# Kernel tuning notes

Measured on AMD Instinct MI355X. Metric: run time of the kernel, lower is better.

Reference implementation:

```python
import jax, jax.numpy as jnp
import numpy as np

D_MODEL = 512
NUM_HEADS = 8
DFF = 2048
DEPTH = D_MODEL // NUM_HEADS
EPS = 1e-6


def setup_inputs() -> dict:
    key = jax.random.key(0)
    ks = jax.random.split(key, 16)
    B, S, d = 4, 2048, D_MODEL
    s = 1.0 / np.sqrt(d)
    inp = {
        'x': jax.random.normal(ks[0], (B, S, d), jnp.float32),
        'Wq': jax.random.normal(ks[1], (d, d), jnp.float32) * s,
        'bq': jnp.zeros((d,), jnp.float32),
        'Wk': jax.random.normal(ks[2], (d, d), jnp.float32) * s,
        'bk': jnp.zeros((d,), jnp.float32),
        'Wv': jax.random.normal(ks[3], (d, d), jnp.float32) * s,
        'bv': jnp.zeros((d,), jnp.float32),
        'Wo': jax.random.normal(ks[4], (d, d), jnp.float32) * s,
        'bo': jnp.zeros((d,), jnp.float32),
        'W1': jax.random.normal(ks[5], (d, DFF), jnp.float32) * s,
        'b1': jnp.zeros((DFF,), jnp.float32),
        'W2': jax.random.normal(ks[6], (DFF, d), jnp.float32) * (1.0 / np.sqrt(DFF)),
        'b2': jnp.zeros((d,), jnp.float32),
        'g1': jnp.ones((d,), jnp.float32),
        'be1': jnp.zeros((d,), jnp.float32),
        'g2': jnp.ones((d,), jnp.float32),
        'be2': jnp.zeros((d,), jnp.float32),
    }
    return inp


def _layer_norm(x, g, b):
    mu = jnp.mean(x, axis=-1, keepdims=True)
    var = jnp.mean(jnp.square(x - mu), axis=-1, keepdims=True)
    return (x - mu) * jax.lax.rsqrt(var + EPS) * g + b


def _split_heads(t, B, S):
    # (B,S,d_model) -> (B,H,S,depth)
    return t.reshape(B, S, NUM_HEADS, DEPTH).transpose(0, 2, 1, 3)


def reference(x, Wq, bq, Wk, bk, Wv, bv, Wo, bo, W1, b1, W2, b2, g1, be1, g2, be2):
    B, S, d = x.shape
    q = _split_heads(x @ Wq + bq, B, S)
    k = _split_heads(x @ Wk + bk, B, S)
    v = _split_heads(x @ Wv + bv, B, S)
    # tf.keras Attention default: UNscaled dot product
    scores = jnp.einsum('bhqd,bhkd->bhqk', q, k)
    attn = jax.nn.softmax(scores, axis=-1)
    ctx = jnp.einsum('bhqk,bhkd->bhqd', attn, v)
    ctx = ctx.transpose(0, 2, 1, 3).reshape(B, S, d)
    attn_out = ctx @ Wo + bo
    x1 = _layer_norm(x + attn_out, g1, be1)
    ff = jax.nn.relu(x1 @ W1 + b1) @ W2 + b2
    return _layer_norm(x1 + ff, g2, be2)
```

## Files before the change

### kernel.cpp

```cpp
#include <hip/hip_runtime.h>
#include <hip/hip_bf16.h>
#include <math.h>

#define NH 8
#define DEPTH 64
#define SEQ 2048
#define BATCH 4
#define DM 512
#define DFFN 2048
#define NROWS (BATCH * SEQ)

typedef __attribute__((ext_vector_type(8))) short  s16x8;
typedef __attribute__((ext_vector_type(4))) short  s16x4;
typedef __attribute__((ext_vector_type(4))) float  f32x4;

__device__ __forceinline__ float bf2f(unsigned short u) {
    union { unsigned int i; float f; } c;
    c.i = ((unsigned int)u) << 16;
    return c.f;
}
__device__ __forceinline__ unsigned short f2bf_rn(float x) {
    union { float f; unsigned int i; } c; c.f = x;
    unsigned int r = c.i + 0x7fffu + ((c.i >> 16) & 1u);
    return (unsigned short)(r >> 16);
}
__device__ __forceinline__ float ldin(const void* p, long i, int f32) {
    return f32 ? ((const float*)p)[i] : bf2f(((const unsigned short*)p)[i]);
}
__device__ __forceinline__ float4 ld4in(const void* p, long i, int f32) {
    if (f32) return *reinterpret_cast<const float4*>((const float*)p + i);
    ushort4 u = *reinterpret_cast<const ushort4*>((const unsigned short*)p + i);
    return make_float4(bf2f(u.x), bf2f(u.y), bf2f(u.z), bf2f(u.w));
}

__global__ void detect_kernel(const void* w, int* flag) {
    if (threadIdx.x == 0 && blockIdx.x == 0) {
        const unsigned short* u = (const unsigned short*)w;
        int isf32 = 0;
        for (int i = 0; i < 2048; ++i) {
            float v = fabsf(bf2f(u[i]));
            if (!(v < 1e3f)) { isf32 = 1; break; }
        }
        *flag = isf32;
    }
}

__global__ __launch_bounds__(256)
void asplit_kernel(const void* __restrict__ A, unsigned short* __restrict__ hi,
                   unsigned short* __restrict__ lo, const int* __restrict__ dflag)
{
    const int f32 = *dflag;
    long i = ((long)blockIdx.x * 256 + threadIdx.x) * 4;
    float4 v = ld4in(A, i, f32);
    float xs[4] = {v.x, v.y, v.z, v.w};
    s16x4 h, l;
    #pragma unroll
    for (int j = 0; j < 4; ++j) {
        unsigned short hh = f2bf_rn(xs[j]);
        h[j] = (short)hh;
        l[j] = (short)f2bf_rn(xs[j] - bf2f(hh));
    }
    *reinterpret_cast<s16x4*>(hi + i) = h;
    *reinterpret_cast<s16x4*>(lo + i) = l;
}

__global__ __launch_bounds__(256)
void wsplit_kernel(const void* __restrict__ W, unsigned short* __restrict__ whiT,
                   unsigned short* __restrict__ wloT, int K, int N,
                   const int* __restrict__ dflag)
{
    const int f32 = *dflag;
    __shared__ float T[64][65];
    const int k0 = blockIdx.x * 64, n0 = blockIdx.y * 64;
    const int tid = threadIdx.x;
    #pragma unroll
    for (int i = 0; i < 4; ++i) {
        int k = (tid >> 4) + i * 16;
        int n = (tid & 15) * 4;
        float4 w4 = ld4in(W, (long)(k0 + k) * N + n0 + n, f32);
        T[k][n] = w4.x; T[k][n + 1] = w4.y; T[k][n + 2] = w4.z; T[k][n + 3] = w4.w;
    }
    __syncthreads();
    #pragma unroll
    for (int i = 0; i < 4; ++i) {
        int n = (tid >> 4) + i * 16;
        int k = (tid & 15) * 4;
        s16x4 hv, lv;
        #pragma unroll
        for (int j = 0; j < 4; ++j) {
            float x = T[k + j][n];
            unsigned short h = f2bf_rn(x);
            hv[j] = (short)h;
            lv[j] = (short)f2bf_rn(x - bf2f(h));
        }
        *reinterpret_cast<s16x4*>(&whiT[(long)(n0 + n) * K + k0 + k]) = hv;
        *reinterpret_cast<s16x4*>(&wloT[(long)(n0 + n) * K + k0 + k]) = lv;
    }
}

__global__ __launch_bounds__(256)
void vtrans_kernel(const unsigned short* __restrict__ vin,
                   unsigned short* __restrict__ vout)
{
    __shared__ unsigned short T[64][72];
    const int tid = threadIdx.x;
    const int s0 = blockIdx.x * 64;
    const int bh = blockIdx.y;
    const unsigned short* src = vin + ((long)bh * SEQ + s0) * DEPTH;
    #pragma unroll
    for (int i = 0; i < 2; ++i) {
        int f = tid + i * 256, row = f >> 3, oct = f & 7;
        *reinterpret_cast<s16x8*>(&T[row][oct * 8]) =
            *reinterpret_cast<const s16x8*>(src + (long)row * DEPTH + oct * 8);
    }
    __syncthreads();
    unsigned short* dst = vout + (long)bh * DEPTH * SEQ + s0;
    #pragma unroll
    for (int i = 0; i < 2; ++i) {
        int f = tid + i * 256;
        int d = f >> 3, oct = f & 7;
        s16x8 v;
        #pragma unroll
        for (int e = 0; e < 8; ++e) v[e] = (short)T[oct * 8 + e][d];
        *reinterpret_cast<s16x8*>(dst + (long)d * SEQ + oct * 8) = v;
    }
}

#define ASTR 40
template<int BM, int AMODE, int OMODE, bool RELU, int TERMS>
__global__ __launch_bounds__(256)
void mfma_gemm(const void* __restrict__ A, const void* __restrict__ A2,
               const unsigned short* __restrict__ WhiT,
               const unsigned short* __restrict__ WloT,
               const void* __restrict__ bias, const void* __restrict__ bias2,
               const void* __restrict__ bias3,
               void* __restrict__ C, void* __restrict__ C2,
               void* __restrict__ C3, void* __restrict__ C4,
               void* __restrict__ C5,
               int M, int N, int K, const int* __restrict__ dflag)
{
    constexpr int FM  = BM / 32;
    constexpr int CPT = BM / 64;
    constexpr int BLO = (TERMS == 3) ? 128 : 1;
    const int f32 = *dflag;
    __shared__ unsigned short Ahi[BM][ASTR], Alo[BM][ASTR];
    __shared__ unsigned short Bhi[128][ASTR];
    __shared__ unsigned short Blo[BLO][ASTR];

    const int tid  = threadIdx.x;
    const int wave = tid >> 6, lane = tid & 63;
    const int lr = lane & 15, lg = lane >> 4;
    const int wm = (wave >> 1) * (BM / 2), wn = (wave & 1) * 64;
    const int bx = blockIdx.x, by = blockIdx.y;

    const int srB = tid >> 1;
    const int shB = (tid & 1) * 16;

    s16x8 arh[CPT], arl[CPT];
    auto loadA = [&](int kt) {
        const unsigned short* ah = (const unsigned short*)A;
        const unsigned short* al = (const unsigned short*)A2;
        #pragma unroll
        for (int i = 0; i < CPT; ++i) {
            int c = tid * CPT + i;
            int row = c >> 2, q = c & 3;
            int gm = by * BM + row;
            int gk = kt + q * 8;
            long base;
            if (AMODE == 3) {
                int b = gm / SEQ, s = gm % SEQ;
                int hh = gk >> 6, dep = gk & 63;
                base = ((long)(b * NH + hh) * SEQ + s) * DEPTH + dep;
            } else {
                base = (long)gm * K + gk;
            }
            arh[i] = *reinterpret_cast<const s16x8*>(ah + base);
            arl[i] = *reinterpret_cast<const s16x8*>(al + base);
        }
    };
    s16x8 brh[2], brl[2];
    auto loadB = [&](int kt) {
        long base = (long)(bx * 128 + srB) * K + kt + shB;
        brh[0] = *reinterpret_cast<const s16x8*>(&WhiT[base]);
        brh[1] = *reinterpret_cast<const s16x8*>(&WhiT[base + 8]);
        if constexpr (TERMS == 3) {
            brl[0] = *reinterpret_cast<const s16x8*>(&WloT[base]);
            brl[1] = *reinterpret_cast<const s16x8*>(&WloT[base + 8]);
        }
    };

    f32x4 acc[FM][4];
    #pragma unroll
    for (int i = 0; i < FM; ++i)
        #pragma unroll
        for (int j = 0; j < 4; ++j) acc[i][j] = (f32x4){0.f, 0.f, 0.f, 0.f};

    loadA(0);
    loadB(0);

    for (int kt = 0; kt < K; kt += 32) {
        #pragma unroll
        for (int i = 0; i < CPT; ++i) {
            int c = tid * CPT + i;
            int row = c >> 2, q = c & 3;
            *reinterpret_cast<s16x8*>(&Ahi[row][q * 8]) = arh[i];
            *reinterpret_cast<s16x8*>(&Alo[row][q * 8]) = arl[i];
        }
        *reinterpret_cast<s16x8*>(&Bhi[srB][shB])     = brh[0];
        *reinterpret_cast<s16x8*>(&Bhi[srB][shB + 8]) = brh[1];
        if constexpr (TERMS == 3) {
            *reinterpret_cast<s16x8*>(&Blo[srB][shB])     = brl[0];
            *reinterpret_cast<s16x8*>(&Blo[srB][shB + 8]) = brl[1];
        }
        __syncthreads();

        if (kt + 32 < K) {
            loadA(kt + 32);
            loadB(kt + 32);
        }

        s16x8 afh[FM], afl[FM], bfh[4], bfl[4];
        #pragma unroll
        for (int f = 0; f < FM; ++f) {
            afh[f] = *reinterpret_cast<const s16x8*>(&Ahi[wm + f * 16 + lr][lg * 8]);
            afl[f] = *reinterpret_cast<const s16x8*>(&Alo[wm + f * 16 + lr][lg * 8]);
        }
        #pragma unroll
        for (int f = 0; f < 4; ++f) {
            bfh[f] = *reinterpret_cast<const s16x8*>(&Bhi[wn + f * 16 + lr][lg * 8]);
            if constexpr (TERMS == 3)
                bfl[f] = *reinterpret_cast<const s16x8*>(&Blo[wn + f * 16 + lr][lg * 8]);
        }
        #pragma unroll
        for (int i = 0; i < FM; ++i)
            #pragma unroll
            for (int j = 0; j < 4; ++j)
                acc[i][j] = __builtin_amdgcn_mfma_f32_16x16x32_bf16(afh[i], bfh[j], acc[i][j], 0, 0, 0);
        #pragma unroll
        for (int i = 0; i < FM; ++i)
            #pragma unroll
            for (int j = 0; j < 4; ++j)
                acc[i][j] = __builtin_amdgcn_mfma_f32_16x16x32_bf16(afl[i], bfh[j], acc[i][j], 0, 0, 0);
        if constexpr (TERMS == 3) {
            #pragma unroll
            for (int i = 0; i < FM; ++i)
                #pragma unroll
                for (int j = 0; j < 4; ++j)
                    acc[i][j] = __builtin_amdgcn_mfma_f32_16x16x32_bf16(afh[i], bfl[j], acc[i][j], 0, 0, 0);
        }
        __syncthreads();
    }

    const int region = bx >> 2;
    #pragma unroll
    for (int fn = 0; fn < 4; ++fn) {
        int gn = bx * 128 + wn + fn * 16 + lr;
        float bv;
        if constexpr (OMODE == 4) {
            const void* bp = (region == 0) ? bias : (region == 1 ? bias2 : bias3);
            bv = ldin(bp, gn & 511, f32);
        } else {
            bv = ldin(bias, gn, f32);
        }
        #pragma unroll
        for (int fm = 0; fm < FM; ++fm) {
            int gm0 = by * BM + wm + fm * 16 + lg * 4;
            #pragma unroll
            for (int r = 0; r < 4; ++r) {
                float vv = acc[fm][fn][r] + bv;
                if (RELU) vv = fmaxf(vv, 0.f);
                int gm = gm0 + r;
                if constexpr (OMODE == 0) {
                    ((float*)C)[(long)gm * N + gn] = vv;
                } else if constexpr (OMODE == 3) {
                    long oi = (long)gm * N + gn;
                    unsigned short h = f2bf_rn(vv);
                    ((unsigned short*)C)[oi] = h;
                    ((unsigned short*)C2)[oi] = f2bf_rn(vv - bf2f(h));
                } else {
                    int b = gm / SEQ, s = gm % SEQ;
                    int hh = (gn & 511) >> 6, dep = gn & 63;
                    long oi = ((long)(b * NH + hh) * SEQ + s) * DEPTH + dep;
                    unsigned short h = f2bf_rn(vv);
                    if (region == 0) {
                        ((unsigned short*)C)[oi]  = h;
                        ((unsigned short*)C2)[oi] = f2bf_rn(vv - bf2f(h));
                    } else if (region == 1) {
                        ((unsigned short*)C3)[oi] = h;
                        ((unsigned short*)C4)[oi] = f2bf_rn(vv - bf2f(h));
                    } else {
                        ((unsigned short*)C5)[oi] = h;
                    }
                }
            }
        }
    }
}

#define KSTR 72
__global__ __launch_bounds__(256)
void attn_kernel2(const unsigned short* __restrict__ Qhi, const unsigned short* __restrict__ Qlo,
                  const unsigned short* __restrict__ Khi_g, const unsigned short* __restrict__ Klo_g,
                  const unsigned short* __restrict__ Vt_g,
                  unsigned short* __restrict__ ctxhi, unsigned short* __restrict__ ctxlo)
{
    __shared__ unsigned short Khi[64][KSTR];
    __shared__ unsigned short Klo[64][KSTR];
    __shared__ unsigned short Vt[64][KSTR];
    __shared__ unsigned short Ps[4][16][KSTR];

    const int tid  = threadIdx.x;
    const int wave = tid >> 6, lane = tid & 63;
    const int lr   = lane & 15;
    const int lg   = lane >> 4;
    const int bh = blockIdx.y;
    const int q0 = blockIdx.x * 64;

    const unsigned short* khb = Khi_g + (long)bh * SEQ * DEPTH;
    const unsigned short* klb = Klo_g + (long)bh * SEQ * DEPTH;
    const unsigned short* vtb = Vt_g + (long)bh * DEPTH * SEQ;

    s16x8 qh8[2], ql8[2];
    {
        const unsigned short* qhp = Qhi + ((long)bh * SEQ + q0 + wave * 16 + lr) * DEPTH + lg * 8;
        const unsigned short* qlp = Qlo + ((long)bh * SEQ + q0 + wave * 16 + lr) * DEPTH + lg * 8;
        #pragma unroll
        for (int c = 0; c < 2; ++c) {
            qh8[c] = *reinterpret_cast<const s16x8*>(qhp + c * 32);
            ql8[c] = *reinterpret_cast<const s16x8*>(qlp + c * 32);
        }
    }

    float m[4], l[4];
    f32x4 o4[4];
    #pragma unroll
    for (int r = 0; r < 4; ++r) { m[r] = -1e30f; l[r] = 0.f; }
    #pragma unroll
    for (int d0 = 0; d0 < 4; ++d0) o4[d0] = (f32x4){0.f, 0.f, 0.f, 0.f};

    for (int kt = 0; kt < SEQ; kt += 64) {
        __syncthreads();
        #pragma unroll
        for (int i = 0; i < 2; ++i) {
            int f = tid + i * 256, row = f >> 3, oct = f & 7;
            *reinterpret_cast<s16x8*>(&Khi[row][oct * 8]) =
                *reinterpret_cast<const s16x8*>(khb + (long)(kt + row) * DEPTH + oct * 8);
            *reinterpret_cast<s16x8*>(&Klo[row][oct * 8]) =
                *reinterpret_cast<const s16x8*>(klb + (long)(kt + row) * DEPTH + oct * 8);
            *reinterpret_cast<s16x8*>(&Vt[row][oct * 8]) =
                *reinterpret_cast<const s16x8*>(vtb + (long)row * SEQ + kt + oct * 8);
        }
        __syncthreads();

        f32x4 s4[4];
        #pragma unroll
        for (int kbl = 0; kbl < 4; ++kbl) {
            f32x4 acc = (f32x4){0.f, 0.f, 0.f, 0.f};
            #pragma unroll
            for (int c = 0; c < 2; ++c) {
                s16x8 kh8 = *reinterpret_cast<const s16x8*>(&Khi[kbl * 16 + lr][c * 32 + lg * 8]);
                s16x8 kl8 = *reinterpret_cast<const s16x8*>(&Klo[kbl * 16 + lr][c * 32 + lg * 8]);
                acc = __builtin_amdgcn_mfma_f32_16x16x32_bf16(qh8[c], kh8, acc, 0, 0, 0);
                acc = __builtin_amdgcn_mfma_f32_16x16x32_bf16(ql8[c], kh8, acc, 0, 0, 0);
                acc = __builtin_amdgcn_mfma_f32_16x16x32_bf16(qh8[c], kl8, acc, 0, 0, 0);
            }
            s4[kbl] = acc;
        }

        #pragma unroll
        for (int r = 0; r < 4; ++r) {
            float mx = fmaxf(fmaxf(s4[0][r], s4[1][r]), fmaxf(s4[2][r], s4[3][r]));
            mx = fmaxf(mx, __shfl_xor(mx, 1));
            mx = fmaxf(mx, __shfl_xor(mx, 2));
            mx = fmaxf(mx, __shfl_xor(mx, 4));
            mx = fmaxf(mx, __shfl_xor(mx, 8));
            float mn = fmaxf(m[r], mx);
            float al = __expf(m[r] - mn);
            m[r] = mn;
            float rs = 0.f;
            #pragma unroll
            for (int kbl = 0; kbl < 4; ++kbl) {
                float p = __expf(s4[kbl][r] - mn);
                rs += p;
                Ps[wave][lg * 4 + r][kbl * 16 + lr] = f2bf_rn(p);
            }
            rs += __shfl_xor(rs, 1);
            rs += __shfl_xor(rs, 2);
            rs += __shfl_xor(rs, 4);
            rs += __shfl_xor(rs, 8);
            l[r] = l[r] * al + rs;
            #pragma unroll
            for (int d0 = 0; d0 < 4; ++d0) o4[d0][r] *= al;
        }

        #pragma unroll
        for (int c = 0; c < 2; ++c) {
            s16x8 p8 = *reinterpret_cast<const s16x8*>(&Ps[wave][lr][c * 32 + lg * 8]);
            #pragma unroll
            for (int d0 = 0; d0 < 4; ++d0) {
                s16x8 v8 = *reinterpret_cast<const s16x8*>(&Vt[d0 * 16 + lr][c * 32 + lg * 8]);
                o4[d0] = __builtin_amdgcn_mfma_f32_16x16x32_bf16(p8, v8, o4[d0], 0, 0, 0);
            }
        }
    }

    unsigned short* chh = ctxhi + (long)bh * SEQ * DEPTH;
    unsigned short* chl = ctxlo + (long)bh * SEQ * DEPTH;
    #pragma unroll
    for (int r = 0; r < 4; ++r) {
        float inv = 1.f / l[r];
        #pragma unroll
        for (int d0 = 0; d0 < 4; ++d0) {
            float val = o4[d0][r] * inv;
            long oi = (long)(q0 + wave * 16 + lg * 4 + r) * DEPTH + d0 * 16 + lr;
            unsigned short h = f2bf_rn(val);
            chh[oi] = h;
            chl[oi] = f2bf_rn(val - bf2f(h));
        }
    }
}

__global__ __launch_bounds__(256)
void attn_f32(const float* __restrict__ q, const float* __restrict__ k,
              const float* __restrict__ v, float* __restrict__ ctx)
{
    __shared__ float Qs[64][68];
    __shared__ float KP[64][68];
    __shared__ float Vs[64][68];
    const int tx = threadIdx.x, ty = threadIdx.y;
    const int tid = ty * 16 + tx;
    const int bh = blockIdx.y;
    const int q0 = blockIdx.x * 64;
    const float* qh = q + (long)bh * SEQ * DEPTH;
    const float* kh = k + (long)bh * SEQ * DEPTH;
    const float* vh = v + (long)bh * SEQ * DEPTH;
    #pragma unroll
    for (int i = 0; i < 4; ++i) {
        int f = tid + i * 256;
        int r = f >> 4, c4 = f & 15;
        float4 qv = *reinterpret_cast<const float4*>(qh + (long)(q0 + r) * DEPTH + c4 * 4);
        Qs[c4 * 4 + 0][r] = qv.x; Qs[c4 * 4 + 1][r] = qv.y;
        Qs[c4 * 4 + 2][r] = qv.z; Qs[c4 * 4 + 3][r] = qv.w;
    }
    float m[4], l[4], o[4][4];
    #pragma unroll
    for (int i = 0; i < 4; ++i) {
        m[i] = -1e30f; l[i] = 0.f;
        #pragma unroll
        for (int j = 0; j < 4; ++j) o[i][j] = 0.f;
    }
    for (int kt = 0; kt < SEQ; kt += 64) {
        __syncthreads();
        #pragma unroll
        for (int i = 0; i < 4; ++i) {
            int f = tid + i * 256;
            int r = f >> 4, c4 = f & 15;
            float4 kv = *reinterpret_cast<const float4*>(kh + (long)(kt + r) * DEPTH + c4 * 4);
            KP[c4 * 4 + 0][r] = kv.x; KP[c4 * 4 + 1][r] = kv.y;
            KP[c4 * 4 + 2][r] = kv.z; KP[c4 * 4 + 3][r] = kv.w;
            float4 vv = *reinterpret_cast<const float4*>(vh + (long)(kt + r) * DEPTH + c4 * 4);
            *reinterpret_cast<float4*>(&Vs[r][c4 * 4]) = vv;
        }
        __syncthreads();
        float sc[4][4] = {};
        #pragma unroll 8
        for (int d = 0; d < 64; ++d) {
            float4 a4 = *reinterpret_cast<const float4*>(&Qs[d][ty * 4]);
            float4 b4 = *reinterpret_cast<const float4*>(&KP[d][tx * 4]);
            float a[4] = {a4.x, a4.y, a4.z, a4.w};
            float b[4] = {b4.x, b4.y, b4.z, b4.w};
            #pragma unroll
            for (int i = 0; i < 4; ++i)
                #pragma unroll
                for (int j = 0; j < 4; ++j)
                    sc[i][j] = fmaf(a[i], b[j], sc[i][j]);
        }
        #pragma unroll
        for (int i = 0; i < 4; ++i) {
            float mx = fmaxf(fmaxf(sc[i][0], sc[i][1]), fmaxf(sc[i][2], sc[i][3]));
            mx = fmaxf(mx, __shfl_xor(mx, 1));
            mx = fmaxf(mx, __shfl_xor(mx, 2));
            mx = fmaxf(mx, __shfl_xor(mx, 4));
            mx = fmaxf(mx, __shfl_xor(mx, 8));
            float mn = fmaxf(m[i], mx);
            float al = __expf(m[i] - mn);
            m[i] = mn;
            float rs = 0.f;
            #pragma unroll
            for (int j = 0; j < 4; ++j) {
                sc[i][j] = __expf(sc[i][j] - mn);
                rs += sc[i][j];
            }
            rs += __shfl_xor(rs, 1);
            rs += __shfl_xor(rs, 2);
            rs += __shfl_xor(rs, 4);
            rs += __shfl_xor(rs, 8);
            l[i] = l[i] * al + rs;
            #pragma unroll
            for (int j = 0; j < 4; ++j) o[i][j] *= al;
        }
        __syncthreads();
        #pragma unroll
        for (int j = 0; j < 4; ++j) {
            float4 pv = make_float4(sc[0][j], sc[1][j], sc[2][j], sc[3][j]);
            *reinterpret_cast<float4*>(&KP[tx * 4 + j][ty * 4]) = pv;
        }
        __syncthreads();
        #pragma unroll 8
        for (int d = 0; d < 64; ++d) {
            float4 p4 = *reinterpret_cast<const float4*>(&KP[d][ty * 4]);
            float4 v4 = *reinterpret_cast<const float4*>(&Vs[d][tx * 4]);
            float p[4] = {p4.x, p4.y, p4.z, p4.w};
            float vv[4] = {v4.x, v4.y, v4.z, v4.w};
            #pragma unroll
            for (int i = 0; i < 4; ++i)
                #pragma unroll
                for (int j = 0; j < 4; ++j)
                    o[i][j] = fmaf(p[i], vv[j], o[i][j]);
        }
    }
    float* ch = ctx + (long)bh * SEQ * DEPTH;
    #pragma unroll
    for (int i = 0; i < 4; ++i) {
        float inv = 1.f / l[i];
        float4 ov = make_float4(o[i][0] * inv, o[i][1] * inv, o[i][2] * inv, o[i][3] * inv);
        *reinterpret_cast<float4*>(&ch[(long)(q0 + ty * 4 + i) * DEPTH + tx * 4]) = ov;
    }
}

template<bool A_INPUT, bool GATHER_IN, bool SPLIT_OUT, bool RELU>
__global__ __launch_bounds__(256)
void gemm_kernel(const void* __restrict__ A,
                 const void* __restrict__ W,
                 const void* __restrict__ bias,
                 float* __restrict__ C,
                 int M, int N, int K, const int* __restrict__ dflag)
{
    const int f32 = *dflag;
    __shared__ float As[16][132];
    __shared__ float Bs[16][68];
    const int tx = threadIdx.x, ty = threadIdx.y;
    const int tid = ty * 16 + tx;
    const int bx = blockIdx.x, by = blockIdx.y;
    const int ca = tid & 3;
    const int ra = tid >> 2;
    const int kb = tid >> 4;
    const int nb = tid & 15;
    auto loadA = [&](int kt, int row) -> float4 {
        int gm = by * 128 + row;
        int gk = kt + ca * 4;
        long base;
        if (GATHER_IN) {
            int b = gm / SEQ, s = gm % SEQ;
            int hh = gk >> 6, dep = gk & 63;
            base = ((long)(b * NH + hh) * SEQ + s) * DEPTH + dep;
        } else {
            base = (long)gm * K + gk;
        }
        if (A_INPUT) return ld4in(A, base, f32);
        return *reinterpret_cast<const float4*>((const float*)A + base);
    };
    auto loadB = [&](int kt) -> float4 {
        return ld4in(W, (long)(kt + kb) * N + bx * 64 + nb * 4, f32);
    };
    float acc[8][4] = {};
    float4 a0 = loadA(0, ra);
    float4 a1 = loadA(0, ra + 64);
    float4 b0 = loadB(0);
    for (int kt = 0; kt < K; kt += 16) {
        As[ca * 4 + 0][ra] = a0.x; As[ca * 4 + 1][ra] = a0.y;
        As[ca * 4 + 2][ra] = a0.z; As[ca * 4 + 3][ra] = a0.w;
        As[ca * 4 + 0][ra + 64] = a1.x; As[ca * 4 + 1][ra + 64] = a1.y;
        As[ca * 4 + 2][ra + 64] = a1.z; As[ca * 4 + 3][ra + 64] = a1.w;
        *reinterpret_cast<float4*>(&Bs[kb][nb * 4]) = b0;
        __syncthreads();
        if (kt + 16 < K) {
            a0 = loadA(kt + 16, ra);
            a1 = loadA(kt + 16, ra + 64);
            b0 = loadB(kt + 16);
        }
        #pragma unroll
        for (int kk = 0; kk < 16; ++kk) {
            float4 x0 = *reinterpret_cast<const float4*>(&As[kk][ty * 8]);
            float4 x1 = *reinterpret_cast<const float4*>(&As[kk][ty * 8 + 4]);
            float4 y0 = *reinterpret_cast<const float4*>(&Bs[kk][tx * 4]);
            float a[8] = {x0.x, x0.y, x0.z, x0.w, x1.x, x1.y, x1.z, x1.w};
            float b[4] = {y0.x, y0.y, y0.z, y0.w};
            #pragma unroll
            for (int i = 0; i < 8; ++i)
                #pragma unroll
                for (int j = 0; j < 4; ++j)
                    acc[i][j] = fmaf(a[i], b[j], acc[i][j]);
        }
        __syncthreads();
    }
    const int gn = bx * 64 + tx * 4;
    float4 bi = ld4in(bias, gn, f32);
    #pragma unroll
    for (int i = 0; i < 8; ++i) {
        int gm = by * 128 + ty * 8 + i;
        float4 v = make_float4(acc[i][0] + bi.x, acc[i][1] + bi.y,
                               acc[i][2] + bi.z, acc[i][3] + bi.w);
        if (RELU) {
            v.x = fmaxf(v.x, 0.f); v.y = fmaxf(v.y, 0.f);
            v.z = fmaxf(v.z, 0.f); v.w = fmaxf(v.w, 0.f);
        }
        long oi;
        if (SPLIT_OUT) {
            int b = gm / SEQ, s = gm % SEQ;
            int hh = gn >> 6, dep = gn & 63;
            oi = ((long)(b * NH + hh) * SEQ + s) * DEPTH + dep;
        } else {
            oi = (long)gm * N + gn;
        }
        *reinterpret_cast<float4*>(C + oi) = v;
    }
}

template<bool A_INPUT, bool FINAL, bool WSPLIT>
__global__ __launch_bounds__(256)
void ln_kernel(const void* __restrict__ a, const float* __restrict__ b,
               const void* __restrict__ g, const void* __restrict__ be,
               void* __restrict__ out, unsigned short* __restrict__ ohi,
               unsigned short* __restrict__ olo, const int* __restrict__ dflag)
{
    const int f32 = *dflag;
    const long row = blockIdx.x;
    const int tid = threadIdx.x;
    const long base = row * DM;

    float v0 = (A_INPUT ? ldin(a, base + tid, f32)       : ((const float*)a)[base + tid])       + b[base + tid];
    float v1 = (A_INPUT ? ldin(a, base + tid + 256, f32) : ((const float*)a)[base + tid + 256]) + b[base + tid + 256];
    float s = v0 + v1;
    float ss = v0 * v0 + v1 * v1;

    #pragma unroll
    for (int off = 32; off > 0; off >>= 1) {
        s  += __shfl_down(s, off);
        ss += __shfl_down(ss, off);
    }
    __shared__ float shs[4], shss[4];
    __shared__ float mean_s, rstd_s;
    const int wid = tid >> 6, lane = tid & 63;
    if (lane == 0) { shs[wid] = s; shss[wid] = ss; }
    __syncthreads();
    if (tid == 0) {
        float S = shs[0] + shs[1] + shs[2] + shs[3];
        float SS = shss[0] + shss[1] + shss[2] + shss[3];
        float mean = S / DM;
        float var = SS / DM - mean * mean;
        mean_s = mean;
        rstd_s = rsqrtf(var + 1e-6f);
    }
    __syncthreads();
    float mean = mean_s, r = rstd_s;

    float o0 = (v0 - mean) * r * ldin(g, tid, f32)       + ldin(be, tid, f32);
    float o1 = (v1 - mean) * r * ldin(g, tid + 256, f32) + ldin(be, tid + 256, f32);
    if (FINAL) {
        if (f32) {
            ((float*)out)[base + tid] = o0;
            ((float*)out)[base + tid + 256] = o1;
        } else {
            ((__hip_bfloat16*)out)[base + tid] = __float2bfloat16(o0);
            ((__hip_bfloat16*)out)[base + tid + 256] = __float2bfloat16(o1);
        }
    } else {
        ((float*)out)[base + tid] = o0;
        ((float*)out)[base + tid + 256] = o1;
    }
    if (WSPLIT) {
        unsigned short h0 = f2bf_rn(o0);
        ohi[base + tid] = h0;
        olo[base + tid] = f2bf_rn(o0 - bf2f(h0));
        unsigned short h1 = f2bf_rn(o1);
        ohi[base + tid + 256] = h1;
        olo[base + tid + 256] = f2bf_rn(o1 - bf2f(h1));
    }
}

extern "C" void kernel_launch(void* const* d_in, const int* in_sizes, int n_in,
                              void* d_out, int out_size, void* d_ws, size_t ws_size,
                              hipStream_t stream)
{
    const void* x   = d_in[0];
    const void* Wq  = d_in[1];
    const void* bq  = d_in[2];
    const void* Wk  = d_in[3];
    const void* bk  = d_in[4];
    const void* Wv  = d_in[5];
    const void* bv  = d_in[6];
    const void* Wo  = d_in[7];
    const void* bo  = d_in[8];
    const void* W1  = d_in[9];
    const void* b1  = d_in[10];
    const void* W2  = d_in[11];
    const void* b2  = d_in[12];
    const void* g1  = d_in[13];
    const void* be1 = d_in[14];
    const void* g2  = d_in[15];
    const void* be2 = d_in[16];

    const size_t MB = 1024ull * 1024;
    char* W = (char*)d_ws;

    unsigned short* xhi  = (unsigned short*)(W + 0 * MB);
    unsigned short* xlo  = (unsigned short*)(W + 8 * MB);
    unsigned short* QhiB = (unsigned short*)(W + 16 * MB);
    unsigned short* QloB = (unsigned short*)(W + 24 * MB);
    unsigned short* KhiB = (unsigned short*)(W + 32 * MB);
    unsigned short* KloB = (unsigned short*)(W + 40 * MB);
    unsigned short* Vrow = (unsigned short*)(W + 48 * MB);
    unsigned short* VtB  = (unsigned short*)(W + 56 * MB);
    unsigned short* cxhi = (unsigned short*)(W + 64 * MB);
    unsigned short* cxlo = (unsigned short*)(W + 72 * MB);
    float* attnout = (float*)(W + 80 * MB);
    float* x1      = (float*)(W + 96 * MB);
    unsigned short* x1hi = cxhi;
    unsigned short* x1lo = cxlo;
    unsigned short* hhi  = (unsigned short*)(W + 0 * MB);
    unsigned short* hlo  = (unsigned short*)(W + 32 * MB);
    float* ffb  = attnout;
    unsigned short* wsp = (unsigned short*)(W + 112 * MB);
    const size_t SW  = (size_t)DM * DM;
    const size_t SW1 = (size_t)DM * DFFN;
    unsigned short* WqkvH = wsp;              unsigned short* WqkvL = WqkvH + 3 * SW;
    unsigned short* WoH = WqkvL + 3 * SW;     unsigned short* WoL = WoH + SW;
    unsigned short* W1H = WoL + SW;           unsigned short* W1L = W1H + SW1;
    unsigned short* W2H = W1L + SW1;          unsigned short* W2L = W2H + SW1;
    int* flag = (int*)(W + 124 * MB);
    const size_t needed = 124 * MB + 16;

    if (ws_size >= needed) {
        detect_kernel<<<1, 64, 0, stream>>>(Wq, flag);

        asplit_kernel<<<(NROWS * DM) / 1024, 256, 0, stream>>>(x, xhi, xlo, flag);
        wsplit_kernel<<<dim3(DM / 64, DM / 64), 256, 0, stream>>>(Wq, WqkvH, WqkvL, DM, DM, flag);
        wsplit_kernel<<<dim3(DM / 64, DM / 64), 256, 0, stream>>>(Wk, WqkvH + SW, WqkvL + SW, DM, DM, flag);
        wsplit_kernel<<<dim3(DM / 64, DM / 64), 256, 0, stream>>>(Wv, WqkvH + 2 * SW, WqkvL + 2 * SW, DM, DM, flag);
        wsplit_kernel<<<dim3(DM / 64, DM / 64), 256, 0, stream>>>(Wo, WoH, WoL, DM, DM, flag);
        wsplit_kernel<<<dim3(DM / 64, DFFN / 64), 256, 0, stream>>>(W1, W1H, W1L, DM, DFFN, flag);
        wsplit_kernel<<<dim3(DFFN / 64, DM / 64), 256, 0, stream>>>(W2, W2H, W2L, DFFN, DM, flag);

        mfma_gemm<128, 2, 4, false, 3><<<dim3(12, NROWS / 128), 256, 0, stream>>>(
            xhi, xlo, WqkvH, WqkvL, bq, bk, bv,
            QhiB, QloB, KhiB, KloB, Vrow, NROWS, 3 * DM, DM, flag);
        vtrans_kernel<<<dim3(SEQ / 64, BATCH * NH), 256, 0, stream>>>(Vrow, VtB);

        attn_kernel2<<<dim3(SEQ / 64, BATCH * NH), 256, 0, stream>>>(
            QhiB, QloB, KhiB, KloB, VtB, cxhi, cxlo);

        mfma_gemm<64, 3, 0, false, 2><<<dim3(4, NROWS / 64), 256, 0, stream>>>(
            cxhi, cxlo, WoH, WoL, bo, nullptr, nullptr,
            attnout, nullptr, nullptr, nullptr, nullptr, NROWS, DM, DM, flag);

        ln_kernel<true, false, true><<<NROWS, 256, 0, stream>>>(
            x, attnout, g1, be1, x1, x1hi, x1lo, flag);

        mfma_gemm<128, 2, 3, true, 2><<<dim3(DFFN / 128, NROWS / 128), 256, 0, stream>>>(
            x1hi, x1lo, W1H, W1L, b1, nullptr, nullptr,
            hhi, hlo, nullptr, nullptr, nullptr, NROWS, DFFN, DM, flag);

        mfma_gemm<64, 2, 0, false, 2><<<dim3(4, NROWS / 64), 256, 0, stream>>>(
            hhi, hlo, W2H, W2L, b2, nullptr, nullptr,
            ffb, nullptr, nullptr, nullptr, nullptr, NROWS, DM, DFFN, flag);

        ln_kernel<false, true, false><<<NROWS, 256, 0, stream>>>(
            x1, ffb, g2, be2, d_out, nullptr, nullptr, flag);
    } else {
        const size_t CH = (size_t)NROWS * DM;
        float* qb   = (float*)d_ws;
        float* kb   = qb + CH;
        float* vb   = kb + CH;
        float* ctx  = vb + CH;
        float* attn = ctx + CH;
        float* x1f  = attn + CH;
        float* hb   = qb;
        float* ffbf = attn;
        int*   flg  = (int*)(qb + 6 * CH);
        dim3 blk(16, 16);
        detect_kernel<<<1, 64, 0, stream>>>(Wq, flg);
        gemm_kernel<true, false, true, false><<<dim3(DM / 64, NROWS / 128), blk, 0, stream>>>(x, Wq, bq, qb, NROWS, DM, DM, flg);
        gemm_kernel<true, false, true, false><<<dim3(DM / 64, NROWS / 128), blk, 0, stream>>>(x, Wk, bk, kb, NROWS, DM, DM, flg);
        gemm_kernel<true, false, true, false><<<dim3(DM / 64, NROWS / 128), blk, 0, stream>>>(x, Wv, bv, vb, NROWS, DM, DM, flg);
        attn_f32<<<dim3(SEQ / 64, BATCH * NH), blk, 0, stream>>>(qb, kb, vb, ctx);
        gemm_kernel<false, true, false, false><<<dim3(DM / 64, NROWS / 128), blk, 0, stream>>>(ctx, Wo, bo, attn, NROWS, DM, DM, flg);
        ln_kernel<true, false, false><<<NROWS, 256, 0, stream>>>(x, attn, g1, be1, x1f, nullptr, nullptr, flg);
        gemm_kernel<false, false, false, true><<<dim3(DFFN / 64, NROWS / 128), blk, 0, stream>>>(x1f, W1, b1, hb, NROWS, DFFN, DM, flg);
        gemm_kernel<false, false, false, false><<<dim3(DM / 64, NROWS / 128), blk, 0, stream>>>(hb, W2, b2, ffbf, NROWS, DM, DFFN, flg);
        ln_kernel<false, true, false><<<NROWS, 256, 0, stream>>>(x1f, ffbf, g2, be2, d_out, nullptr, nullptr, flg);
    }
}
```

Baseline: 471.2 us.

## Use exp2 softmax with prescaled Q, MFMA row sums, wave-per-row LayerNorm

Pre-scales Wq and bq by log2(e) during the weight split so attention can call the hardware exp2 directly instead of __expf. Replaces the per-row shuffle reductions of softmax sums with an MFMA of the bf16 probabilities against a ones vector. This also makes the denominator use the same rounded bf16 P values as the numerator. Rewrites LayerNorm to process one row per wave with float4 loads and stores, removing shared memory and block barriers.

```diff
diff --git a/kernel.cpp b/kernel.cpp
--- a/kernel.cpp
+++ b/kernel.cpp
@@ -9,6 +9,9 @@
 #define DM 512
 #define DFFN 2048
 #define NROWS (BATCH * SEQ)
+#define LOG2E 1.44269504088896f
+
+#define EXP2F(x) __builtin_amdgcn_exp2f(x)
 
 typedef __attribute__((ext_vector_type(8))) short  s16x8;
 typedef __attribute__((ext_vector_type(4))) short  s16x4;
@@ -66,7 +69,7 @@
 
 __global__ __launch_bounds__(256)
 void wsplit_kernel(const void* __restrict__ W, unsigned short* __restrict__ whiT,
-                   unsigned short* __restrict__ wloT, int K, int N,
+                   unsigned short* __restrict__ wloT, int K, int N, float scale,
                    const int* __restrict__ dflag)
 {
     const int f32 = *dflag;
@@ -78,7 +81,8 @@
         int k = (tid >> 4) + i * 16;
         int n = (tid & 15) * 4;
         float4 w4 = ld4in(W, (long)(k0 + k) * N + n0 + n, f32);
-        T[k][n] = w4.x; T[k][n + 1] = w4.y; T[k][n + 2] = w4.z; T[k][n + 3] = w4.w;
+        T[k][n] = w4.x * scale; T[k][n + 1] = w4.y * scale;
+        T[k][n + 2] = w4.z * scale; T[k][n + 3] = w4.w * scale;
     }
     __syncthreads();
     #pragma unroll
@@ -259,6 +263,7 @@
         if constexpr (OMODE == 4) {
             const void* bp = (region == 0) ? bias : (region == 1 ? bias2 : bias3);
             bv = ldin(bp, gn & 511, f32);
+            if (region == 0) bv *= LOG2E;
         } else {
             bv = ldin(bias, gn, f32);
         }
@@ -316,6 +321,9 @@
     const int bh = blockIdx.y;
     const int q0 = blockIdx.x * 64;
 
+    const s16x8 ones8 = {(short)0x3F80, (short)0x3F80, (short)0x3F80, (short)0x3F80,
+                         (short)0x3F80, (short)0x3F80, (short)0x3F80, (short)0x3F80};
+
     const unsigned short* khb = Khi_g + (long)bh * SEQ * DEPTH;
     const unsigned short* klb = Klo_g + (long)bh * SEQ * DEPTH;
     const unsigned short* vtb = Vt_g + (long)bh * DEPTH * SEQ;
@@ -331,10 +339,11 @@
         }
     }
 
-    float m[4], l[4];
+    float m[4];
+    f32x4 lacc = (f32x4){0.f, 0.f, 0.f, 0.f};
     f32x4 o4[4];
     #pragma unroll
-    for (int r = 0; r < 4; ++r) { m[r] = -1e30f; l[r] = 0.f; }
+    for (int r = 0; r < 4; ++r) m[r] = -1e30f;
     #pragma unroll
     for (int d0 = 0; d0 < 4; ++d0) o4[d0] = (f32x4){0.f, 0.f, 0.f, 0.f};
 
@@ -375,27 +384,25 @@
             mx = fmaxf(mx, __shfl_xor(mx, 4));
             mx = fmaxf(mx, __shfl_xor(mx, 8));
             float mn = fmaxf(m[r], mx);
-            float al = __expf(m[r] - mn);
+            float al = EXP2F(m[r] - mn);
             m[r] = mn;
-            float rs = 0.f;
-            #pragma unroll
-            for (int kbl = 0; kbl < 4; ++kbl) {
-                float p = __expf(s4[kbl][r] - mn);
-                rs += p;
-                Ps[wave][lg * 4 + r][kbl * 16 + lr] = f2bf_rn(p);
-            }
-            rs += __shfl_xor(rs, 1);
-            rs += __shfl_xor(rs, 2);
-            rs += __shfl_xor(rs, 4);
-            rs += __shfl_xor(rs, 8);
-            l[r] = l[r] * al + rs;
-            #pragma unroll
-            for (int d0 = 0; d0 < 4; ++d0) o4[d0][r] *= al;
+            float p0 = EXP2F(s4[0][r] - mn);
+            float p1 = EXP2F(s4[1][r] - mn);
+            float p2 = EXP2F(s4[2][r] - mn);
+            float p3 = EXP2F(s4[3][r] - mn);
+            unsigned short* pr = &Ps[wave][lg * 4 + r][lr];
+            pr[0]  = f2bf_rn(p0);
+            pr[16] = f2bf_rn(p1);
+            pr[32] = f2bf_rn(p2);
+            pr[48] = f2bf_rn(p3);
+            lacc[r] *= al;
+            o4[0][r] *= al; o4[1][r] *= al; o4[2][r] *= al; o4[3][r] *= al;
         }
 
         #pragma unroll
         for (int c = 0; c < 2; ++c) {
             s16x8 p8 = *reinterpret_cast<const s16x8*>(&Ps[wave][lr][c * 32 + lg * 8]);
+            lacc = __builtin_amdgcn_mfma_f32_16x16x32_bf16(p8, ones8, lacc, 0, 0, 0);
             #pragma unroll
             for (int d0 = 0; d0 < 4; ++d0) {
                 s16x8 v8 = *reinterpret_cast<const s16x8*>(&Vt[d0 * 16 + lr][c * 32 + lg * 8]);
@@ -408,7 +415,7 @@
     unsigned short* chl = ctxlo + (long)bh * SEQ * DEPTH;
     #pragma unroll
     for (int r = 0; r < 4; ++r) {
-        float inv = 1.f / l[r];
+        float inv = 1.f / lacc[r];
         #pragma unroll
         for (int d0 = 0; d0 < 4; ++d0) {
             float val = o4[d0][r] * inv;
@@ -625,57 +632,62 @@
                unsigned short* __restrict__ olo, const int* __restrict__ dflag)
 {
     const int f32 = *dflag;
-    const long row = blockIdx.x;
-    const int tid = threadIdx.x;
+    const int wave = threadIdx.x >> 6, lane = threadIdx.x & 63;
+    const long row = (long)blockIdx.x * 4 + wave;
     const long base = row * DM;
-
-    float v0 = (A_INPUT ? ldin(a, base + tid, f32)       : ((const float*)a)[base + tid])       + b[base + tid];
-    float v1 = (A_INPUT ? ldin(a, base + tid + 256, f32) : ((const float*)a)[base + tid + 256]) + b[base + tid + 256];
-    float s = v0 + v1;
-    float ss = v0 * v0 + v1 * v1;
-
-    #pragma unroll
-    for (int off = 32; off > 0; off >>= 1) {
-        s  += __shfl_down(s, off);
-        ss += __shfl_down(ss, off);
-    }
-    __shared__ float shs[4], shss[4];
-    __shared__ float mean_s, rstd_s;
-    const int wid = tid >> 6, lane = tid & 63;
-    if (lane == 0) { shs[wid] = s; shss[wid] = ss; }
-    __syncthreads();
-    if (tid == 0) {
-        float S = shs[0] + shs[1] + shs[2] + shs[3];
-        float SS = shss[0] + shss[1] + shss[2] + shss[3];
-        float mean = S / DM;
-        float var = SS / DM - mean * mean;
-        mean_s = mean;
-        rstd_s = rsqrtf(var + 1e-6f);
-    }
-    __syncthreads();
-    float mean = mean_s, r = rstd_s;
-
-    float o0 = (v0 - mean) * r * ldin(g, tid, f32)       + ldin(be, tid, f32);
-    float o1 = (v1 - mean) * r * ldin(g, tid + 256, f32) + ldin(be, tid + 256, f32);
-    if (FINAL) {
-        if (f32) {
-            ((float*)out)[base + tid] = o0;
-            ((float*)out)[base + tid + 256] = o1;
-        } else {
-            ((__hip_bfloat16*)out)[base + tid] = __float2bfloat16(o0);
-            ((__hip_bfloat16*)out)[base + tid + 256] = __float2bfloat16(o1);
-        }
+    const int i0 = lane * 4, i1 = 256 + lane * 4;
+
+    float4 a0 = A_INPUT ? ld4in(a, base + i0, f32)
+                        : *reinterpret_cast<const float4*>((const float*)a + base + i0);
+    float4 a1 = A_INPUT ? ld4in(a, base + i1, f32)
+                        : *reinterpret_cast<const float4*>((const float*)a + base + i1);
+    float4 b0 = *reinterpret_cast<const float4*>(b + base + i0);
+    float4 b1 = *reinterpret_cast<const float4*>(b + base + i1);
+    float v[8] = {a0.x + b0.x, a0.y + b0.y, a0.z + b0.z, a0.w + b0.w,
+                  a1.x + b1.x, a1.y + b1.y, a1.z + b1.z, a1.w + b1.w};
+    float s = 0.f, ss = 0.f;
+    #pragma unroll
+    for (int j = 0; j < 8; ++j) { s += v[j]; ss += v[j] * v[j]; }
+    #pragma unroll
+    for (int off = 1; off < 64; off <<= 1) {
+        s  += __shfl_xor(s, off);
+        ss += __shfl_xor(ss, off);
+    }
+    float mean = s / DM;
+    float var = ss / DM - mean * mean;
+    float rr = rsqrtf(var + 1e-6f);
+
+    float4 g0 = ld4in(g, i0, f32), g1 = ld4in(g, i1, f32);
+    float4 e0 = ld4in(be, i0, f32), e1 = ld4in(be, i1, f32);
+    float gg[8] = {g0.x, g0.y, g0.z, g0.w, g1.x, g1.y, g1.z, g1.w};
+    float ee[8] = {e0.x, e0.y, e0.z, e0.w, e1.x, e1.y, e1.z, e1.w};
+    float o[8];
+    #pragma unroll
+    for (int j = 0; j < 8; ++j) o[j] = (v[j] - mean) * rr * gg[j] + ee[j];
+
+    if (FINAL && !f32) {
+        s16x4 u0, u1;
+        #pragma unroll
+        for (int j = 0; j < 4; ++j) { u0[j] = (short)f2bf_rn(o[j]); u1[j] = (short)f2bf_rn(o[4 + j]); }
+        *reinterpret_cast<s16x4*>((unsigned short*)out + base + i0) = u0;
+        *reinterpret_cast<s16x4*>((unsigned short*)out + base + i1) = u1;
     } else {
-        ((float*)out)[base + tid] = o0;
-        ((float*)out)[base + tid + 256] = o1;
+        *reinterpret_cast<float4*>((float*)out + base + i0) = make_float4(o[0], o[1], o[2], o[3]);
+        *reinterpret_cast<float4*>((float*)out + base + i1) = make_float4(o[4], o[5], o[6], o[7]);
     }
     if (WSPLIT) {
-        unsigned short h0 = f2bf_rn(o0);
-        ohi[base + tid] = h0;
-        olo[base + tid] = f2bf_rn(o0 - bf2f(h0));
-        unsigned short h1 = f2bf_rn(o1);
-        ohi[base + tid + 256] = h1;
-        olo[base + tid + 256] = f2bf_rn(o1 - bf2f(h1));
+        s16x4 h0, l0, h1, l1;
+        #pragma unroll
+        for (int j = 0; j < 4; ++j) {
+            unsigned short h = f2bf_rn(o[j]);
+            h0[j] = (short)h; l0[j] = (short)f2bf_rn(o[j] - bf2f(h));
+            unsigned short hb = f2bf_rn(o[4 + j]);
+            h1[j] = (short)hb; l1[j] = (short)f2bf_rn(o[4 + j] - bf2f(hb));
+        }
+        *reinterpret_cast<s16x4*>(ohi + base + i0) = h0;
+        *reinterpret_cast<s16x4*>(olo + base + i0) = l0;
+        *reinterpret_cast<s16x4*>(ohi + base + i1) = h1;
+        *reinterpret_cast<s16x4*>(olo + base + i1) = l1;
     }
 }
 
@@ -735,12 +747,12 @@
         detect_kernel<<<1, 64, 0, stream>>>(Wq, flag);
 
         asplit_kernel<<<(NROWS * DM) / 1024, 256, 0, stream>>>(x, xhi, xlo, flag);
-        wsplit_kernel<<<dim3(DM / 64, DM / 64), 256, 0, stream>>>(Wq, WqkvH, WqkvL, DM, DM, flag);
-        wsplit_kernel<<<dim3(DM / 64, DM / 64), 256, 0, stream>>>(Wk, WqkvH + SW, WqkvL + SW, DM, DM, flag);
-        wsplit_kernel<<<dim3(DM / 64, DM / 64), 256, 0, stream>>>(Wv, WqkvH + 2 * SW, WqkvL + 2 * SW, DM, DM, flag);
-        wsplit_kernel<<<dim3(DM / 64, DM / 64), 256, 0, stream>>>(Wo, WoH, WoL, DM, DM, flag);
-        wsplit_kernel<<<dim3(DM / 64, DFFN / 64), 256, 0, stream>>>(W1, W1H, W1L, DM, DFFN, flag);
-        wsplit_kernel<<<dim3(DFFN / 64, DM / 64), 256, 0, stream>>>(W2, W2H, W2L, DFFN, DM, flag);
+        wsplit_kernel<<<dim3(DM / 64, DM / 64), 256, 0, stream>>>(Wq, WqkvH, WqkvL, DM, DM, LOG2E, flag);
+        wsplit_kernel<<<dim3(DM / 64, DM / 64), 256, 0, stream>>>(Wk, WqkvH + SW, WqkvL + SW, DM, DM, 1.f, flag);
+        wsplit_kernel<<<dim3(DM / 64, DM / 64), 256, 0, stream>>>(Wv, WqkvH + 2 * SW, WqkvL + 2 * SW, DM, DM, 1.f, flag);
+        wsplit_kernel<<<dim3(DM / 64, DM / 64), 256, 0, stream>>>(Wo, WoH, WoL, DM, DM, 1.f, flag);
+        wsplit_kernel<<<dim3(DM / 64, DFFN / 64), 256, 0, stream>>>(W1, W1H, W1L, DM, DFFN, 1.f, flag);
+        wsplit_kernel<<<dim3(DFFN / 64, DM / 64), 256, 0, stream>>>(W2, W2H, W2L, DFFN, DM, 1.f, flag);
 
         mfma_gemm<128, 2, 4, false, 3><<<dim3(12, NROWS / 128), 256, 0, stream>>>(
             xhi, xlo, WqkvH, WqkvL, bq, bk, bv,
@@ -754,7 +766,7 @@
             cxhi, cxlo, WoH, WoL, bo, nullptr, nullptr,
             attnout, nullptr, nullptr, nullptr, nullptr, NROWS, DM, DM, flag);
 
-        ln_kernel<true, false, true><<<NROWS, 256, 0, stream>>>(
+        ln_kernel<true, false, true><<<NROWS / 4, 256, 0, stream>>>(
             x, attnout, g1, be1, x1, x1hi, x1lo, flag);
 
         mfma_gemm<128, 2, 3, true, 2><<<dim3(DFFN / 128, NROWS / 128), 256, 0, stream>>>(
@@ -765,7 +777,7 @@
             hhi, hlo, W2H, W2L, b2, nullptr, nullptr,
             ffb, nullptr, nullptr, nullptr, nullptr, NROWS, DM, DFFN, flag);
 
-        ln_kernel<false, true, false><<<NROWS, 256, 0, stream>>>(
+        ln_kernel<false, true, false><<<NROWS / 4, 256, 0, stream>>>(
             x1, ffb, g2, be2, d_out, nullptr, nullptr, flag);
     } else {
         const size_t CH = (size_t)NROWS * DM;
@@ -785,9 +797,9 @@
         gemm_kernel<true, false, true, false><<<dim3(DM / 64, NROWS / 128), blk, 0, stream>>>(x, Wv, bv, vb, NROWS, DM, DM, flg);
         attn_f32<<<dim3(SEQ / 64, BATCH * NH), blk, 0, stream>>>(qb, kb, vb, ctx);
         gemm_kernel<false, true, false, false><<<dim3(DM / 64, NROWS / 128), blk, 0, stream>>>(ctx, Wo, bo, attn, NROWS, DM, DM, flg);
-        ln_kernel<true, false, false><<<NROWS, 256, 0, stream>>>(x, attn, g1, be1, x1f, nullptr, nullptr, flg);
+        ln_kernel<true, false, false><<<NROWS / 4, 256, 0, stream>>>(x, attn, g1, be1, x1f, nullptr, nullptr, flg);
         gemm_kernel<false, false, false, true><<<dim3(DFFN / 64, NROWS / 128), blk, 0, stream>>>(x1f, W1, b1, hb, NROWS, DFFN, DM, flg);
         gemm_kernel<false, false, false, false><<<dim3(DM / 64, NROWS / 128), blk, 0, stream>>>(hb, W2, b2, ffbf, NROWS, DM, DFFN, flg);
-        ln_kernel<false, true, false><<<NROWS, 256, 0, stream>>>(x1f, ffbf, g2, be2, d_out, nullptr, nullptr, flg);
-    }
-}
+        ln_kernel<false, true, false><<<NROWS / 4, 256, 0, stream>>>(x1f, ffbf, g2, be2, d_out, nullptr, nullptr, flg);
+    }
+}
```

Result: faster. 448.7 us (-4.8%).
